# Performance work log

Measured on AMD Instinct MI355X. Metric: run time of the kernel, lower is better.

Reference implementation:

```python
import jax, jax.numpy as jnp
import numpy as np

THETA = 10000.0


def _apply_rope(xh, positions, theta):
    # xh: [B, H, S, d_k]; positions: [S] int
    d_k = xh.shape[-1]
    inv_freq = theta ** (-jnp.arange(0, d_k, 2, dtype=jnp.float32) / d_k)  # [d_k/2]
    angles = positions.astype(jnp.float32)[:, None] * inv_freq[None, :]     # [S, d_k/2]
    cos = jnp.cos(angles)
    sin = jnp.sin(angles)
    x1 = xh[..., 0::2]
    x2 = xh[..., 1::2]
    r1 = x1 * cos - x2 * sin
    r2 = x1 * sin + x2 * cos
    return jnp.stack([r1, r2], axis=-1).reshape(xh.shape)


def setup_inputs() -> dict:
    key = jax.random.key(0)
    ks = jax.random.split(key, 5)
    B, S, D = 2, 2048, 1024
    std = np.sqrt(1.0 / D).astype(np.float32)
    return {
        "x": jax.random.normal(ks[0], (B, S, D), dtype=jnp.float32),
        "token_positions": jnp.arange(S, dtype=jnp.int64 if jax.config.jax_enable_x64 else jnp.int32),
        "Wq": jax.random.normal(ks[1], (D, D), dtype=jnp.float32) * std,
        "Wk": jax.random.normal(ks[2], (D, D), dtype=jnp.float32) * std,
        "Wv": jax.random.normal(ks[3], (D, D), dtype=jnp.float32) * std,
        "Wo": jax.random.normal(ks[4], (D, D), dtype=jnp.float32) * std,
    }


def reference(x, token_positions, Wq, Wk, Wv, Wo):
    B, S, D = x.shape
    n_heads = 16
    d_k = D // n_heads

    # QKV projections (torch does x @ W.T)
    q = x @ Wq.T
    k = x @ Wk.T
    v = x @ Wv.T

    def split_heads(t):  # [B,S,D] -> [B,H,S,d_k]
        return t.reshape(B, S, n_heads, d_k).transpose(0, 2, 1, 3)

    qh = _apply_rope(split_heads(q), token_positions, THETA)
    kh = _apply_rope(split_heads(k), token_positions, THETA)
    vh = split_heads(v)

    scores = jnp.einsum("bhqd,bhkd->bhqk", qh, kh) / jnp.sqrt(jnp.float32(d_k))
    causal = jnp.tril(jnp.ones((S, S), dtype=bool))
    scores = jnp.where(causal, scores, -jnp.inf)
    attn = jax.nn.softmax(scores, axis=-1)

    out_h = jnp.einsum("bhqk,bhkd->bhqd", attn, vh)  # [B,H,S,d_k]
    out = out_h.transpose(0, 2, 1, 3).reshape(B, S, D)
    return out @ Wo.T
```

## Files before the change

kernel.cpp:

```cpp
#include <hip/hip_runtime.h>

typedef unsigned int u32;
typedef __attribute__((ext_vector_type(8))) short short8;
typedef __attribute__((ext_vector_type(4))) float f32x4;

__device__ __forceinline__ unsigned short f2bf(float f) {
  union { float f; u32 u; } x; x.f = f;
  u32 u = x.u;
  return (unsigned short)((u + 0x7fffu + ((u >> 16) & 1u)) >> 16);
}
__device__ __forceinline__ float bf2f(unsigned short b) {
  union { u32 u; float f; } x; x.u = ((u32)b) << 16;
  return x.f;
}
__device__ __forceinline__ f32x4 mfma_bf16(short8 a, short8 b, f32x4 c) {
  return __builtin_amdgcn_mfma_f32_16x16x32_bf16(a, b, c, 0, 0, 0);
}

typedef __attribute__((address_space(3))) unsigned int lds_u32;
typedef const __attribute__((address_space(1))) unsigned int glb_u32;
__device__ __forceinline__ void gload_lds16(const unsigned short* g, unsigned short* l) {
  __builtin_amdgcn_global_load_lds((glb_u32*)g, (lds_u32*)l, 16, 0, 0);
}

__global__ __launch_bounds__(256) void cvt_kernel(const float* __restrict__ src,
                                                  unsigned short* __restrict__ dst, int n4) {
  int i = blockIdx.x * 256 + threadIdx.x;
  if (i >= n4) return;
  float4 v = ((const float4*)src)[i];
  ushort4 o;
  o.x = f2bf(v.x); o.y = f2bf(v.y); o.z = f2bf(v.z); o.w = f2bf(v.w);
  ((ushort4*)dst)[i] = o;
}

__global__ __launch_bounds__(256) void cvt_w_kernel(const float* __restrict__ wq,
                                                    const float* __restrict__ wk,
                                                    const float* __restrict__ wv,
                                                    const float* __restrict__ wo,
                                                    unsigned short* __restrict__ dqkv,
                                                    unsigned short* __restrict__ dwo) {
  const int i = blockIdx.x * 256 + threadIdx.x;
  const int w = blockIdx.y;
  const float* src = (w == 0) ? wq : (w == 1) ? wk : (w == 2) ? wv : wo;
  unsigned short* dst = (w == 3) ? dwo : dqkv + (size_t)w * 1048576;
  float4 v = ((const float4*)src)[i];
  ushort4 o;
  o.x = f2bf(v.x); o.y = f2bf(v.y); o.z = f2bf(v.z); o.w = f2bf(v.w);
  ((ushort4*)dst)[i] = o;
}

__global__ __launch_bounds__(256) void gemm_qkv(const unsigned short* __restrict__ A,
                                                const unsigned short* __restrict__ B,
                                                unsigned short* __restrict__ qk,
                                                unsigned short* __restrict__ kk,
                                                unsigned short* __restrict__ vtm) {
  constexpr int K = 1024;
  __shared__ unsigned short As[128 * 32];
  __shared__ unsigned short Bs[128 * 32];
  const int tid = threadIdx.x;
  const int wave = tid >> 6, lane = tid & 63;
  const int l15 = lane & 15, quad = lane >> 4;
  const int wr = wave >> 1, wc = wave & 1;
  const int m0 = blockIdx.y * 128, n0 = blockIdx.x * 128;
  f32x4 acc[4][4] = {};
  const int srow = wave * 32 + (lane >> 2);
  const int scol = (lane & 3) * 8;
  const unsigned short* Ag0 = A + (size_t)(m0 + srow) * K + scol;
  const unsigned short* Ag1 = A + (size_t)(m0 + srow + 16) * K + scol;
  const unsigned short* Bg0 = B + (size_t)(n0 + srow) * K + scol;
  const unsigned short* Bg1 = B + (size_t)(n0 + srow + 16) * K + scol;
  unsigned short* Al0 = &As[wave * 1024];
  unsigned short* Al1 = &As[wave * 1024 + 512];
  unsigned short* Bl0 = &Bs[wave * 1024];
  unsigned short* Bl1 = &Bs[wave * 1024 + 512];
  for (int k0 = 0; k0 < K; k0 += 32) {
    __syncthreads();
    gload_lds16(Ag0 + k0, Al0);
    gload_lds16(Ag1 + k0, Al1);
    gload_lds16(Bg0 + k0, Bl0);
    gload_lds16(Bg1 + k0, Bl1);
    __syncthreads();
    short8 a[4], b[4];
#pragma unroll
    for (int i = 0; i < 4; ++i) a[i] = *(const short8*)&As[(wr * 64 + i * 16 + l15) * 32 + quad * 8];
#pragma unroll
    for (int j = 0; j < 4; ++j) b[j] = *(const short8*)&Bs[(wc * 64 + j * 16 + l15) * 32 + quad * 8];
#pragma unroll
    for (int i = 0; i < 4; ++i)
#pragma unroll
      for (int j = 0; j < 4; ++j) acc[i][j] = mfma_bf16(a[i], b[j], acc[i][j]);
  }
  const int proj = n0 >> 10;
  const int nn0 = (n0 & 1023) + wc * 64;
  if (proj < 2) {
    unsigned short* dst = (proj == 0) ? qk : kk;
#pragma unroll
    for (int i = 0; i < 4; ++i) {
      const int mb = m0 + wr * 64 + i * 16 + quad * 4;
#pragma unroll
      for (int j = 0; j < 4; ++j) {
        const int nn = nn0 + j * 16 + l15;
#pragma unroll
        for (int r = 0; r < 4; ++r) dst[(size_t)(mb + r) * 1024 + nn] = f2bf(acc[i][j][r]);
      }
    }
  } else {
#pragma unroll
    for (int i = 0; i < 4; ++i) {
      const int mb = m0 + wr * 64 + i * 16 + quad * 4;
      const int bb = mb >> 11, s = mb & 2047;
#pragma unroll
      for (int j = 0; j < 4; ++j) {
        const int nn = nn0 + j * 16 + l15;
        const int h = nn >> 6, d = nn & 63;
        ushort4 v4;
        v4.x = f2bf(acc[i][j][0]); v4.y = f2bf(acc[i][j][1]);
        v4.z = f2bf(acc[i][j][2]); v4.w = f2bf(acc[i][j][3]);
        *(ushort4*)&vtm[(((size_t)bb * 16 + h) * 64 + d) * 2048 + s] = v4;
      }
    }
  }
}

__global__ __launch_bounds__(256) void rope_kernel(unsigned short* __restrict__ q,
                                                   unsigned short* __restrict__ k,
                                                   const int* __restrict__ pos) {
  const int idx = blockIdx.x * 256 + threadIdx.x;
  const int i = idx & 31;
  const int h = (idx >> 5) & 15;
  const int s = (idx >> 9) & 2047;
  const int b = idx >> 20;
  const float p = (float)pos[s];
  const float inv = exp2f(-0.4152410118609203f * (float)i);
  float sn, cs;
  sincosf(p * inv, &sn, &cs);
  const size_t base = ((size_t)(b * 2048 + s)) * 1024 + h * 64 + 2 * i;
  {
    u32* qp = (u32*)(q + base);
    u32 w = *qp;
    float x1 = bf2f((unsigned short)(w & 0xffff)), x2 = bf2f((unsigned short)(w >> 16));
    *qp = (u32)f2bf(x1 * cs - x2 * sn) | ((u32)f2bf(x1 * sn + x2 * cs) << 16);
  }
  {
    u32* kp = (u32*)(k + base);
    u32 w = *kp;
    float x1 = bf2f((unsigned short)(w & 0xffff)), x2 = bf2f((unsigned short)(w >> 16));
    *kp = (u32)f2bf(x1 * cs - x2 * sn) | ((u32)f2bf(x1 * sn + x2 * cs) << 16);
  }
}

__global__ __launch_bounds__(256) void attn_shared(const unsigned short* __restrict__ qk,
                                                   const unsigned short* __restrict__ kk,
                                                   const unsigned short* __restrict__ vtm,
                                                   unsigned short* __restrict__ om) {
  __shared__ unsigned short Ks[64 * 64];
  __shared__ unsigned short Vs[64 * 64];
  __shared__ unsigned short PlA[4][32 * 72];
  const int tid = threadIdx.x;
  const int wave = tid >> 6, lane = tid & 63;
  const int l15 = lane & 15, quad = lane >> 4;
  unsigned short* Pl = PlA[wave];
  const int bid = blockIdx.x;
  const int bh = bid & 31;
  const int qblk = 15 - (bid >> 5);
  const int b = bh >> 4, h = bh & 15;
  const int qbase = qblk * 128 + wave * 32;
  const unsigned short* Qp = qk + (size_t)b * 2048 * 1024 + h * 64;
  const unsigned short* Kp = kk + (size_t)b * 2048 * 1024 + h * 64;
  const unsigned short* Vp = vtm + (size_t)bh * 64 * 2048;
  short8 qf[2][2];
#pragma unroll
  for (int f = 0; f < 2; ++f)
#pragma unroll
    for (int hh = 0; hh < 2; ++hh)
      qf[f][hh] = *(const short8*)(Qp + (size_t)(qbase + f * 16 + l15) * 1024 + hh * 32 + quad * 8);
  f32x4 o4[2][4] = {};
  f32x4 ls[2] = {};
  short8 ones;
#pragma unroll
  for (int j = 0; j < 8; ++j) ones[j] = (short)0x3F80;
  const float SC = 0.18033688011112042f;
  const int nkb = (qblk * 128 + 191) >> 6;
  const int nkw = (qbase + 95) >> 6;
  const int srow = wave * 16 + (lane >> 3);
  const int scs = (((lane & 7) ^ (srow & 7)) * 8);
  const unsigned short* KgB = Kp + (size_t)srow * 1024 + scs;
  const unsigned short* VgB = Vp + (size_t)srow * 2048 + scs;
  unsigned short* Kl0 = &Ks[(wave * 16) * 64];
  unsigned short* Kl1 = &Ks[(wave * 16 + 8) * 64];
  unsigned short* Vl0 = &Vs[(wave * 16) * 64];
  unsigned short* Vl1 = &Vs[(wave * 16 + 8) * 64];
  const int sw0 = ((quad ^ (l15 & 7)) * 8);
  const int sw1 = (((4 + quad) ^ (l15 & 7)) * 8);
  for (int kt = 0; kt < nkb; ++kt) {
    const int kbase = kt << 6;
    __syncthreads();
    gload_lds16(KgB + (size_t)kbase * 1024, Kl0);
    gload_lds16(KgB + (size_t)kbase * 1024 + 8 * 1024, Kl1);
    gload_lds16(VgB + kbase, Vl0);
    gload_lds16(VgB + kbase + 8 * 2048, Vl1);
    __syncthreads();
    if (kt < nkw) {
      short8 kb[4][2], vb[4][2];
#pragma unroll
      for (int nt = 0; nt < 4; ++nt) {
        kb[nt][0] = *(const short8*)&Ks[(nt * 16 + l15) * 64 + sw0];
        kb[nt][1] = *(const short8*)&Ks[(nt * 16 + l15) * 64 + sw1];
      }
#pragma unroll
      for (int t = 0; t < 4; ++t) {
        vb[t][0] = *(const short8*)&Vs[(t * 16 + l15) * 64 + sw0];
        vb[t][1] = *(const short8*)&Vs[(t * 16 + l15) * 64 + sw1];
      }
      f32x4 s4[2][4] = {};
#pragma unroll
      for (int f = 0; f < 2; ++f)
#pragma unroll
        for (int nt = 0; nt < 4; ++nt) {
          s4[f][nt] = mfma_bf16(qf[f][0], kb[nt][0], s4[f][nt]);
          s4[f][nt] = mfma_bf16(qf[f][1], kb[nt][1], s4[f][nt]);
        }
      const bool edge = (kbase + 63 > qbase);
#pragma unroll
      for (int f = 0; f < 2; ++f) {
        const int row0 = qbase + f * 16 + quad * 4;
#pragma unroll
        for (int nt = 0; nt < 4; ++nt) {
          const int col = kbase + nt * 16 + l15;
#pragma unroll
          for (int r = 0; r < 4; ++r) {
            float p = exp2f(s4[f][nt][r] * SC);
            if (edge && col > row0 + r) p = 0.f;
            Pl[(f * 16 + quad * 4 + r) * 72 + nt * 16 + l15] = f2bf(p);
          }
        }
      }
      __asm volatile("s_waitcnt lgkmcnt(0)" ::: "memory");
      short8 pa[2][2];
#pragma unroll
      for (int f = 0; f < 2; ++f)
#pragma unroll
        for (int hh = 0; hh < 2; ++hh)
          pa[f][hh] = *(const short8*)&Pl[(f * 16 + l15) * 72 + hh * 32 + quad * 8];
#pragma unroll
      for (int f = 0; f < 2; ++f) {
#pragma unroll
        for (int t = 0; t < 4; ++t) {
          o4[f][t] = mfma_bf16(pa[f][0], vb[t][0], o4[f][t]);
          o4[f][t] = mfma_bf16(pa[f][1], vb[t][1], o4[f][t]);
        }
        ls[f] = mfma_bf16(pa[f][0], ones, ls[f]);
        ls[f] = mfma_bf16(pa[f][1], ones, ls[f]);
      }
    }
  }
#pragma unroll
  for (int f = 0; f < 2; ++f) {
    f32x4 rl;
#pragma unroll
    for (int r = 0; r < 4; ++r) rl[r] = 1.f / ls[f][r];
#pragma unroll
    for (int t = 0; t < 4; ++t)
#pragma unroll
      for (int r = 0; r < 4; ++r) {
        const int srw = qbase + f * 16 + quad * 4 + r;
        om[((size_t)b * 2048 + srw) * 1024 + h * 64 + t * 16 + l15] = f2bf(o4[f][t][r] * rl[r]);
      }
  }
}

__global__ __launch_bounds__(256) void gemm_out(const unsigned short* __restrict__ A,
                                                const unsigned short* __restrict__ B,
                                                float* __restrict__ C) {
  constexpr int K = 1024;
  __shared__ unsigned short As[64 * 32];
  __shared__ unsigned short Bs[128 * 32];
  const int tid = threadIdx.x;
  const int wave = tid >> 6, lane = tid & 63;
  const int l15 = lane & 15, quad = lane >> 4;
  const int m0 = blockIdx.y * 64, n0 = blockIdx.x * 128;
  f32x4 acc[4][2] = {};
  const int lr = lane >> 2, lc = (lane & 3) * 8;
  const unsigned short* Ag  = A + (size_t)(m0 + wave * 16 + lr) * K + lc;
  const unsigned short* Bg0 = B + (size_t)(n0 + wave * 32 + lr) * K + lc;
  const unsigned short* Bg1 = B + (size_t)(n0 + wave * 32 + 16 + lr) * K + lc;
  unsigned short* Al  = &As[wave * 512];
  unsigned short* Bl0 = &Bs[wave * 1024];
  unsigned short* Bl1 = &Bs[wave * 1024 + 512];
  for (int k0 = 0; k0 < K; k0 += 32) {
    __syncthreads();
    gload_lds16(Ag + k0, Al);
    gload_lds16(Bg0 + k0, Bl0);
    gload_lds16(Bg1 + k0, Bl1);
    __syncthreads();
    short8 a[4], b[2];
#pragma unroll
    for (int i = 0; i < 4; ++i) a[i] = *(const short8*)&As[(i * 16 + l15) * 32 + quad * 8];
#pragma unroll
    for (int j = 0; j < 2; ++j) b[j] = *(const short8*)&Bs[(wave * 32 + j * 16 + l15) * 32 + quad * 8];
#pragma unroll
    for (int i = 0; i < 4; ++i)
#pragma unroll
      for (int j = 0; j < 2; ++j) acc[i][j] = mfma_bf16(a[i], b[j], acc[i][j]);
  }
#pragma unroll
  for (int i = 0; i < 4; ++i)
#pragma unroll
    for (int j = 0; j < 2; ++j)
#pragma unroll
      for (int r = 0; r < 4; ++r)
        C[(size_t)(m0 + i * 16 + quad * 4 + r) * 1024 + n0 + wave * 32 + j * 16 + l15] =
            acc[i][j][r];
}

extern "C" void kernel_launch(void* const* d_in, const int* in_sizes, int n_in,
                              void* d_out, int out_size, void* d_ws, size_t ws_size,
                              hipStream_t stream) {
  const float* x  = (const float*)d_in[0];
  const int* pos  = (const int*)d_in[1];
  const float* Wq = (const float*)d_in[2];
  const float* Wk = (const float*)d_in[3];
  const float* Wv = (const float*)d_in[4];
  const float* Wo = (const float*)d_in[5];
  float* out = (float*)d_out;
  char* ws = (char*)d_ws;
  unsigned short* xb   = (unsigned short*)(ws);
  unsigned short* wqkv = (unsigned short*)(ws + (size_t)( 8 << 20));
  unsigned short* wob  = (unsigned short*)(ws + (size_t)(14 << 20));
  unsigned short* qkb  = (unsigned short*)(ws + (size_t)(16 << 20));
  unsigned short* kkb  = (unsigned short*)(ws + (size_t)(24 << 20));
  unsigned short* vtm  = (unsigned short*)(ws + (size_t)(32 << 20));
  unsigned short* om   = (unsigned short*)(ws + (size_t)(40 << 20));

  const int NX4 = 4096 * 1024 / 4;
  hipLaunchKernelGGL(cvt_kernel, dim3(NX4 / 256), dim3(256), 0, stream, x, xb, NX4);
  hipLaunchKernelGGL(cvt_w_kernel, dim3(1024, 4), dim3(256), 0, stream, Wq, Wk, Wv, Wo, wqkv, wob);

  hipLaunchKernelGGL(gemm_qkv, dim3(24, 32), dim3(256), 0, stream, xb, wqkv, qkb, kkb, vtm);
  hipLaunchKernelGGL(rope_kernel, dim3(8192), dim3(256), 0, stream, qkb, kkb, pos);
  hipLaunchKernelGGL(attn_shared, dim3(512), dim3(256), 0, stream, qkb, kkb, vtm, om);
  hipLaunchKernelGGL(gemm_out, dim3(8, 64), dim3(256), 0, stream, om, wob, out);
}
```

Before: 231.1 us.

## Double-buffer LDS tiles in QKV GEMM, attention and output GEMM

Each of the three main kernels now keeps two LDS buffers per operand. The next K/V or A/B tile is issued with global_load_lds before the current tile is consumed, and one barrier per iteration replaces the previous pair. The aim is to overlap global-to-LDS transfer latency with the MFMA work and to halve barrier count. The cost is doubled LDS footprint, most notably in the attention kernel, which may reduce the number of resident workgroups per CU.

New measurement: 258.9 us. 1.12x slower.

```diff
diff --git a/kernel.cpp b/kernel.cpp
--- a/kernel.cpp
+++ b/kernel.cpp
@@ -55,8 +55,8 @@
                                                 unsigned short* __restrict__ kk,
                                                 unsigned short* __restrict__ vtm) {
   constexpr int K = 1024;
-  __shared__ unsigned short As[128 * 32];
-  __shared__ unsigned short Bs[128 * 32];
+  __shared__ unsigned short As[2][128 * 32];
+  __shared__ unsigned short Bs[2][128 * 32];
   const int tid = threadIdx.x;
   const int wave = tid >> 6, lane = tid & 63;
   const int l15 = lane & 15, quad = lane >> 4;
@@ -69,27 +69,33 @@
   const unsigned short* Ag1 = A + (size_t)(m0 + srow + 16) * K + scol;
   const unsigned short* Bg0 = B + (size_t)(n0 + srow) * K + scol;
   const unsigned short* Bg1 = B + (size_t)(n0 + srow + 16) * K + scol;
-  unsigned short* Al0 = &As[wave * 1024];
-  unsigned short* Al1 = &As[wave * 1024 + 512];
-  unsigned short* Bl0 = &Bs[wave * 1024];
-  unsigned short* Bl1 = &Bs[wave * 1024 + 512];
+#define QKV_STAGE(c, k0)                                \
+  do {                                                  \
+    gload_lds16(Ag0 + (k0), &As[c][wave * 1024]);       \
+    gload_lds16(Ag1 + (k0), &As[c][wave * 1024 + 512]); \
+    gload_lds16(Bg0 + (k0), &Bs[c][wave * 1024]);       \
+    gload_lds16(Bg1 + (k0), &Bs[c][wave * 1024 + 512]); \
+  } while (0)
+  QKV_STAGE(0, 0);
+  __syncthreads();
+  int cur = 0;
   for (int k0 = 0; k0 < K; k0 += 32) {
+    if (k0 + 32 < K) QKV_STAGE(cur ^ 1, k0 + 32);
+    short8 a[4], b[4];
+#pragma unroll
+    for (int i = 0; i < 4; ++i)
+      a[i] = *(const short8*)&As[cur][(wr * 64 + i * 16 + l15) * 32 + quad * 8];
+#pragma unroll
+    for (int j = 0; j < 4; ++j)
+      b[j] = *(const short8*)&Bs[cur][(wc * 64 + j * 16 + l15) * 32 + quad * 8];
+#pragma unroll
+    for (int i = 0; i < 4; ++i)
+#pragma unroll
+      for (int j = 0; j < 4; ++j) acc[i][j] = mfma_bf16(a[i], b[j], acc[i][j]);
     __syncthreads();
-    gload_lds16(Ag0 + k0, Al0);
-    gload_lds16(Ag1 + k0, Al1);
-    gload_lds16(Bg0 + k0, Bl0);
-    gload_lds16(Bg1 + k0, Bl1);
-    __syncthreads();
-    short8 a[4], b[4];
-#pragma unroll
-    for (int i = 0; i < 4; ++i) a[i] = *(const short8*)&As[(wr * 64 + i * 16 + l15) * 32 + quad * 8];
-#pragma unroll
-    for (int j = 0; j < 4; ++j) b[j] = *(const short8*)&Bs[(wc * 64 + j * 16 + l15) * 32 + quad * 8];
-#pragma unroll
-    for (int i = 0; i < 4; ++i)
-#pragma unroll
-      for (int j = 0; j < 4; ++j) acc[i][j] = mfma_bf16(a[i], b[j], acc[i][j]);
-  }
+    cur ^= 1;
+  }
+#undef QKV_STAGE
   const int proj = n0 >> 10;
   const int nn0 = (n0 & 1023) + wc * 64;
   if (proj < 2) {
@@ -153,8 +159,8 @@
                                                    const unsigned short* __restrict__ kk,
                                                    const unsigned short* __restrict__ vtm,
                                                    unsigned short* __restrict__ om) {
-  __shared__ unsigned short Ks[64 * 64];
-  __shared__ unsigned short Vs[64 * 64];
+  __shared__ unsigned short Ks[2][64 * 64];
+  __shared__ unsigned short Vs[2][64 * 64];
   __shared__ unsigned short PlA[4][32 * 72];
   const int tid = threadIdx.x;
   const int wave = tid >> 6, lane = tid & 63;
@@ -186,31 +192,33 @@
   const int scs = (((lane & 7) ^ (srow & 7)) * 8);
   const unsigned short* KgB = Kp + (size_t)srow * 1024 + scs;
   const unsigned short* VgB = Vp + (size_t)srow * 2048 + scs;
-  unsigned short* Kl0 = &Ks[(wave * 16) * 64];
-  unsigned short* Kl1 = &Ks[(wave * 16 + 8) * 64];
-  unsigned short* Vl0 = &Vs[(wave * 16) * 64];
-  unsigned short* Vl1 = &Vs[(wave * 16 + 8) * 64];
   const int sw0 = ((quad ^ (l15 & 7)) * 8);
   const int sw1 = (((4 + quad) ^ (l15 & 7)) * 8);
+#define ATTN_STAGE(c, kb)                                                    \
+  do {                                                                       \
+    gload_lds16(KgB + (size_t)(kb) * 1024, &Ks[c][(wave * 16) * 64]);        \
+    gload_lds16(KgB + (size_t)(kb) * 1024 + 8 * 1024,                        \
+                &Ks[c][(wave * 16 + 8) * 64]);                               \
+    gload_lds16(VgB + (kb), &Vs[c][(wave * 16) * 64]);                       \
+    gload_lds16(VgB + (kb) + 8 * 2048, &Vs[c][(wave * 16 + 8) * 64]);        \
+  } while (0)
+  ATTN_STAGE(0, 0);
+  __syncthreads();
+  int cur = 0;
   for (int kt = 0; kt < nkb; ++kt) {
-    const int kbase = kt << 6;
-    __syncthreads();
-    gload_lds16(KgB + (size_t)kbase * 1024, Kl0);
-    gload_lds16(KgB + (size_t)kbase * 1024 + 8 * 1024, Kl1);
-    gload_lds16(VgB + kbase, Vl0);
-    gload_lds16(VgB + kbase + 8 * 2048, Vl1);
-    __syncthreads();
+    if (kt + 1 < nkb) ATTN_STAGE(cur ^ 1, (kt + 1) << 6);
     if (kt < nkw) {
+      const int kbase = kt << 6;
       short8 kb[4][2], vb[4][2];
 #pragma unroll
       for (int nt = 0; nt < 4; ++nt) {
-        kb[nt][0] = *(const short8*)&Ks[(nt * 16 + l15) * 64 + sw0];
-        kb[nt][1] = *(const short8*)&Ks[(nt * 16 + l15) * 64 + sw1];
+        kb[nt][0] = *(const short8*)&Ks[cur][(nt * 16 + l15) * 64 + sw0];
+        kb[nt][1] = *(const short8*)&Ks[cur][(nt * 16 + l15) * 64 + sw1];
       }
 #pragma unroll
       for (int t = 0; t < 4; ++t) {
-        vb[t][0] = *(const short8*)&Vs[(t * 16 + l15) * 64 + sw0];
-        vb[t][1] = *(const short8*)&Vs[(t * 16 + l15) * 64 + sw1];
+        vb[t][0] = *(const short8*)&Vs[cur][(t * 16 + l15) * 64 + sw0];
+        vb[t][1] = *(const short8*)&Vs[cur][(t * 16 + l15) * 64 + sw1];
       }
       f32x4 s4[2][4] = {};
 #pragma unroll
@@ -253,7 +261,10 @@
         ls[f] = mfma_bf16(pa[f][1], ones, ls[f]);
       }
     }
-  }
+    __syncthreads();
+    cur ^= 1;
+  }
+#undef ATTN_STAGE
 #pragma unroll
   for (int f = 0; f < 2; ++f) {
     f32x4 rl;
@@ -273,8 +284,8 @@
                                                 const unsigned short* __restrict__ B,
                                                 float* __restrict__ C) {
   constexpr int K = 1024;
-  __shared__ unsigned short As[64 * 32];
-  __shared__ unsigned short Bs[128 * 32];
+  __shared__ unsigned short As[2][64 * 32];
+  __shared__ unsigned short Bs[2][128 * 32];
   const int tid = threadIdx.x;
   const int wave = tid >> 6, lane = tid & 63;
   const int l15 = lane & 15, quad = lane >> 4;
@@ -284,25 +295,31 @@
   const unsigned short* Ag  = A + (size_t)(m0 + wave * 16 + lr) * K + lc;
   const unsigned short* Bg0 = B + (size_t)(n0 + wave * 32 + lr) * K + lc;
   const unsigned short* Bg1 = B + (size_t)(n0 + wave * 32 + 16 + lr) * K + lc;
-  unsigned short* Al  = &As[wave * 512];
-  unsigned short* Bl0 = &Bs[wave * 1024];
-  unsigned short* Bl1 = &Bs[wave * 1024 + 512];
+#define OUT_STAGE(c, k0)                                \
+  do {                                                  \
+    gload_lds16(Ag + (k0), &As[c][wave * 512]);         \
+    gload_lds16(Bg0 + (k0), &Bs[c][wave * 1024]);       \
+    gload_lds16(Bg1 + (k0), &Bs[c][wave * 1024 + 512]); \
+  } while (0)
+  OUT_STAGE(0, 0);
+  __syncthreads();
+  int cur = 0;
   for (int k0 = 0; k0 < K; k0 += 32) {
+    if (k0 + 32 < K) OUT_STAGE(cur ^ 1, k0 + 32);
+    short8 a[4], b[2];
+#pragma unroll
+    for (int i = 0; i < 4; ++i) a[i] = *(const short8*)&As[cur][(i * 16 + l15) * 32 + quad * 8];
+#pragma unroll
+    for (int j = 0; j < 2; ++j)
+      b[j] = *(const short8*)&Bs[cur][(wave * 32 + j * 16 + l15) * 32 + quad * 8];
+#pragma unroll
+    for (int i = 0; i < 4; ++i)
+#pragma unroll
+      for (int j = 0; j < 2; ++j) acc[i][j] = mfma_bf16(a[i], b[j], acc[i][j]);
     __syncthreads();
-    gload_lds16(Ag + k0, Al);
-    gload_lds16(Bg0 + k0, Bl0);
-    gload_lds16(Bg1 + k0, Bl1);
-    __syncthreads();
-    short8 a[4], b[2];
-#pragma unroll
-    for (int i = 0; i < 4; ++i) a[i] = *(const short8*)&As[(i * 16 + l15) * 32 + quad * 8];
-#pragma unroll
-    for (int j = 0; j < 2; ++j) b[j] = *(const short8*)&Bs[(wave * 32 + j * 16 + l15) * 32 + quad * 8];
-#pragma unroll
-    for (int i = 0; i < 4; ++i)
-#pragma unroll
-      for (int j = 0; j < 2; ++j) acc[i][j] = mfma_bf16(a[i], b[j], acc[i][j]);
-  }
+    cur ^= 1;
+  }
+#undef OUT_STAGE
 #pragma unroll
   for (int i = 0; i < 4; ++i)
 #pragma unroll
```
